# Optimization experiments

Hardware: AMD Instinct MI355X
Metric: run time of the kernel (lower is better)

Reference implementation:

```python
import jax, jax.numpy as jnp
import numpy as np

B, T, C, N = 4, 1024, 1024, 64
H = C // N
# dims = [max(32, 32*round(fac*C**p/32))] per module formula for C=1024
D_W, D_A, D_V, D_G = 64, 64, 32, 160
GN_EPS = 0.00064


def setup_inputs() -> dict:
    key = jax.random.key(0)
    keys = iter(jax.random.split(key, 40))

    def rn(shape, s=0.02):
        return jax.random.normal(next(keys), shape, jnp.float32) * s

    return {
        "x": jax.random.normal(next(keys), (B, T, C), jnp.float32),
        "v_first": jax.random.normal(next(keys), (B, T, C), jnp.float32),
        "x_r": rn((1, 1, C), 0.5), "x_w": rn((1, 1, C), 0.5), "x_k": rn((1, 1, C), 0.5),
        "x_v": rn((1, 1, C), 0.5), "x_a": rn((1, 1, C), 0.5), "x_g": rn((1, 1, C), 0.5),
        "w0": rn((1, 1, C), 0.5) - 1.0, "w1": rn((C, D_W)), "w2": rn((D_W, C)),
        "a0": rn((1, 1, C), 0.5), "a1": rn((C, D_A)), "a2": rn((D_A, C)),
        "v0p": rn((1, 1, C), 0.5), "v1": rn((C, D_V)), "v2": rn((D_V, C)),
        "g1": rn((C, D_G)), "g2": rn((D_G, C)),
        "k_k": rn((1, 1, C), 0.2) + 0.8, "k_a": rn((1, 1, C), 0.2) + 1.0,
        "r_k": rn((H, N), 0.5),
        "W_r": rn((C, C)), "W_k": rn((C, C)), "W_v": rn((C, C)), "W_o": rn((C, C)),
        "gn_w": jnp.ones((C,), jnp.float32), "gn_b": jnp.zeros((C,), jnp.float32),
    }


def _group_norm(x2, wgt, bias):
    # torch GroupNorm(H groups, C channels) on [B*T, C]: normalize each N-chunk
    xg = x2.reshape(x2.shape[0], H, N)
    mu = xg.mean(-1, keepdims=True)
    var = ((xg - mu) ** 2).mean(-1, keepdims=True)  # biased var, as torch
    xn = (xg - mu) * jax.lax.rsqrt(var + GN_EPS)
    return xn.reshape(x2.shape) * wgt + bias


def rwkv7_recurrence(r, w, k, v, a, b):
    # RWKV-7 chunked-cuda semantics (wind_rwkv naive reference), all [B,T,H,N];
    # w is the per-channel decay exp(-exp(w_raw)) in (0,1).
    # state s: [B,H,N,N], s[i,j] ~ value_i x key_j
    # s_t = s_{t-1} * diag(w_t) + (s_{t-1} @ a_t) outer b_t + v_t outer k_t
    # y_t = s_t @ r_t
    def step(s, inp):
        r_t, w_t, k_t, v_t, a_t, b_t = inp  # each [B,H,N]
        sa = jnp.einsum('bhij,bhj->bhi', s, a_t)
        s = (s * w_t[:, :, None, :]
             + sa[..., None] * b_t[:, :, None, :]
             + v_t[..., None] * k_t[:, :, None, :])
        y = jnp.einsum('bhij,bhj->bhi', s, r_t)
        return s, y

    xs = tuple(jnp.swapaxes(t, 0, 1) for t in (r, w, k, v, a, b))  # [T,B,H,N]
    s0 = jnp.zeros((r.shape[0], r.shape[2], r.shape[3], r.shape[3]), r.dtype)
    _, ys = jax.lax.scan(step, s0, xs)
    return jnp.swapaxes(ys, 0, 1)  # [B,T,H,N]


def reference(x, v_first, x_r, x_w, x_k, x_v, x_a, x_g, w0, w1, w2, a0, a1, a2,
              v0p, v1, v2, g1, g2, k_k, k_a, r_k, W_r, W_k, W_v, W_o, gn_w, gn_b):
    Bx, Tx, Cx = x.shape
    # F.pad(x, (0,0,1,-1)): shift tokens right by one, zero at t=0
    last_x = jnp.concatenate([jnp.zeros_like(x[:, :1]), x[:, :-1]], axis=1)
    dx = last_x - x
    xr, xw, xk, xv, xa, xg = (x + m * dx for m in (x_r, x_w, x_k, x_v, x_a, x_g))
    r = xr @ W_r.T
    w = -jax.nn.softplus(-w0 - jnp.tanh(xw @ w1) @ w2) - 0.5
    k = xk @ W_k.T
    v = xv @ W_v.T
    v = v + (v_first - v) * jax.nn.sigmoid(v0p + (xv @ v1) @ v2)
    a = jax.nn.sigmoid(a0 + (xa @ a1) @ a2)
    g = jax.nn.sigmoid(xg @ g1) @ g2
    kk = k * k_k
    k = k * (1.0 + (a - 1.0) * k_a)
    rs, ws, ks, vs, kks, aa = (t.reshape(Bx, Tx, H, N) for t in (r, w, k, v, kk, a))
    # F.normalize(kk, dim=-1) with eps clamp 1e-12
    kks = kks / jnp.maximum(jnp.linalg.norm(kks, axis=-1, keepdims=True), 1e-12)
    wdec = jnp.exp(-jnp.exp(ws))
    y = rwkv7_recurrence(rs, wdec, ks, vs, kks, -kks * aa)  # [B,T,H,N]
    yn = _group_norm(y.reshape(Bx * Tx, Cx), gn_w, gn_b).reshape(Bx, Tx, Cx)
    yn = yn + ((rs * ks * r_k).sum(-1, keepdims=True) * vs).reshape(Bx, Tx, Cx)
    return (yn * g) @ W_o.T
```

## Files before the change

kernel.cpp:

```cpp
#include <hip/hip_runtime.h>
#include <hip/hip_bf16.h>
#include <math.h>


using bf16 = __hip_bfloat16;
typedef __attribute__((ext_vector_type(8))) short bf16x8;
typedef __attribute__((ext_vector_type(4))) float f32x4;

#define DEVINL __device__ __forceinline__

DEVINL float b2f(bf16 v) { return __bfloat162float(v); }
DEVINL bf16 f2b(float f) { return __float2bfloat16(f); }
DEVINL float sigm(float x) { return 1.f / (1.f + __expf(-x)); }
DEVINL float bfbits2f(unsigned short s) { return __uint_as_float(((unsigned)s) << 16); }
DEVINL float lo16(unsigned u) { return __uint_as_float(u << 16); }
DEVINL float hi16(unsigned u) { return __uint_as_float(u & 0xffff0000u); }
DEVINL float ldin(const void* p, size_t i, int fl) {
  return fl ? ((const float*)p)[i] : b2f(((const bf16*)p)[i]);
}

DEVINL void g2lds16(const void* g, void* l) {
  __builtin_amdgcn_global_load_lds(
      (__attribute__((address_space(1))) void*)(g),
      (__attribute__((address_space(3))) void*)(l), 16, 0, 0);
}

template<int CTRL>
DEVINL float dpp_add(float x) {
  int t = __builtin_amdgcn_update_dpp(0, __float_as_int(x), CTRL, 0xf, 0xf, true);
  return x + __int_as_float(t);
}
DEVINL float rowsum16(float x) {
  x = dpp_add<0x121>(x);
  x = dpp_add<0x122>(x);
  x = dpp_add<0x124>(x);
  x = dpp_add<0x128>(x);
  return x;
}

DEVINL size_t stream_sb(int row, int h) {
  return ((size_t)((row >> 10) * 16 + h) * 1024 + (row & 1023)) * 512;
}

__global__ void detect_kernel(const unsigned* __restrict__ x, int* __restrict__ flag) {
  __shared__ int cnt[4];
  int tid = threadIdx.x;
  unsigned w = x[tid];
  float v = fabsf(bfbits2f((unsigned short)(w & 0xffffu)));
  bool plaus = (v >= 1e-4f && v <= 16.f);
  unsigned long long m = __ballot(plaus);
  if ((tid & 63) == 0) cnt[tid >> 6] = __popcll(m);
  __syncthreads();
  if (tid == 0) *flag = (cnt[0] + cnt[1] + cnt[2] + cnt[3] < 128) ? 1 : 0;
}

__global__ __launch_bounds__(256)
void prep_kernel(const void* __restrict__ x,
    const void* mr, const void* mw, const void* mk,
    const void* mv, const void* ma, const void* mg,
    const void* W_r, const void* W_k, const void* W_v, const void* W_o,
    bf16* cWr, bf16* cWk, bf16* cWv, bf16* cWo,
    const void* w1, const void* w2, const void* a1, const void* a2,
    const void* v1, const void* v2, const void* g1, const void* g2,
    bf16* w1t, bf16* w2t, bf16* a1t, bf16* a2t,
    bf16* v1t, bf16* v2t, bf16* g1t, bf16* g2t,
    const int* __restrict__ flag,
    bf16* oxr, bf16* oxw, bf16* oxk, bf16* oxv, bf16* oxa, bf16* oxg)
{
  int fl = *flag;
  int bx = blockIdx.x;
  if (bx < 16384) {
    size_t idx = (size_t)bx * 256 + threadIdx.x;
    int c = (int)(idx & 1023);
    int t = (int)((idx >> 10) & 1023);
    float xc = ldin(x, idx, fl);
    float px = (t == 0) ? 0.f : ldin(x, idx - 1024, fl);
    float dx = px - xc;
    oxr[idx] = f2b(xc + ldin(mr, c, fl) * dx);
    oxw[idx] = f2b(xc + ldin(mw, c, fl) * dx);
    oxk[idx] = f2b(xc + ldin(mk, c, fl) * dx);
    oxv[idx] = f2b(xc + ldin(mv, c, fl) * dx);
    oxa[idx] = f2b(xc + ldin(ma, c, fl) * dx);
    oxg[idx] = f2b(xc + ldin(mg, c, fl) * dx);
  } else if (bx < 32768) {
    int g = (bx - 16384) * 256 + threadIdx.x;
    int seg = g >> 20, i = g & 1048575;
    const void* s = seg == 0 ? W_r : seg == 1 ? W_k : seg == 2 ? W_v : W_o;
    bf16* d = seg == 0 ? cWr : seg == 1 ? cWk : seg == 2 ? cWv : cWo;
    d[i] = fl ? f2b(((const float*)s)[i]) : ((const bf16*)s)[i];
  } else {
    int idx = (bx - 32768) * 256 + threadIdx.x;
    if (idx >= 655360) return;
    const int ends[8] = {65536, 131072, 196608, 262144, 294912, 327680, 491520, 655360};
    const int Ks[8] = {1024, 64, 1024, 64, 1024, 32, 1024, 160};
    const int Nd[8] = {64, 1024, 64, 1024, 32, 1024, 160, 1024};
    const void* srcs[8] = {w1, w2, a1, a2, v1, v2, g1, g2};
    bf16* dsts[8] = {w1t, w2t, a1t, a2t, v1t, v2t, g1t, g2t};
    int seg = 0, start = 0;
#pragma unroll
    for (int s2 = 0; s2 < 7; s2++)
      if (idx >= ends[s2]) { seg = s2 + 1; start = ends[s2]; }
    int local = idx - start;
    int K = Ks[seg], N = Nd[seg];
    int k = local / N, n = local - k * N;
    dsts[seg][(size_t)n * K + k] = f2b(ldin(srcs[seg], local, fl));
  }
}

template<typename Epi>
DEVINL void gemm_core(const bf16* __restrict__ A, const bf16* __restrict__ Bt,
                      int K, int Brows, int m0, int n0, Epi&& epi)
{
  __shared__ short As[128 * 32];
  __shared__ short Bs[128 * 32];
  const int tid = threadIdx.x;
  const int wid = tid >> 6, lane = tid & 63;
  const int wr = (wid >> 1) * 64, wc = (wid & 1) * 64;

  f32x4 acc[4][4] = {};

  const int lrow = lane >> 2;
  const int lcol = (lane & 3) * 8;
  int arow0 = m0 + (wid * 2 + 0) * 16 + lrow;
  int arow1 = m0 + (wid * 2 + 1) * 16 + lrow;
  int brow0 = n0 + (wid * 2 + 0) * 16 + lrow; if (brow0 >= Brows) brow0 = Brows - 1;
  int brow1 = n0 + (wid * 2 + 1) * 16 + lrow; if (brow1 >= Brows) brow1 = Brows - 1;

  const short* Ag = (const short*)A;
  const short* Bg = (const short*)Bt;

  for (int kk = 0; kk < K; kk += 32) {
    __syncthreads();
    g2lds16(Ag + (size_t)arow0 * K + kk + lcol, As + (wid * 2 + 0) * 512);
    g2lds16(Ag + (size_t)arow1 * K + kk + lcol, As + (wid * 2 + 1) * 512);
    g2lds16(Bg + (size_t)brow0 * K + kk + lcol, Bs + (wid * 2 + 0) * 512);
    g2lds16(Bg + (size_t)brow1 * K + kk + lcol, Bs + (wid * 2 + 1) * 512);
    __syncthreads();
    bf16x8 af[4], bfr[4];
#pragma unroll
    for (int mi = 0; mi < 4; mi++)
      af[mi] = *(const bf16x8*)(As + (wr + mi * 16 + (lane & 15)) * 32 + (lane >> 4) * 8);
#pragma unroll
    for (int ni = 0; ni < 4; ni++)
      bfr[ni] = *(const bf16x8*)(Bs + (wc + ni * 16 + (lane & 15)) * 32 + (lane >> 4) * 8);
#pragma unroll
    for (int mi = 0; mi < 4; mi++)
#pragma unroll
      for (int ni = 0; ni < 4; ni++)
        acc[mi][ni] = __builtin_amdgcn_mfma_f32_16x16x32_bf16(af[mi], bfr[ni], acc[mi][ni], 0, 0, 0);
  }

  const int cl0 = lane & 15, r0 = (lane >> 4) * 4;
#pragma unroll
  for (int mi = 0; mi < 4; mi++)
#pragma unroll
    for (int ni = 0; ni < 4; ni++) {
      int col = n0 + wc + ni * 16 + cl0;
#pragma unroll
      for (int rr = 0; rr < 4; rr++)
        epi(m0 + wr + mi * 16 + r0 + rr, col, acc[mi][ni][rr]);
    }
}

__global__ __launch_bounds__(256)
void stage1_kernel(const bf16* xw, const bf16* xa, const bf16* xv, const bf16* xg,
                   const bf16* w1t, const bf16* a1t, const bf16* v1t, const bf16* g1t,
                   bf16* hw, bf16* ha, bf16* hv, bf16* hg)
{
  int y = blockIdx.y;
  int seg = (y <= 2) ? y : 3;
  int n0 = (y == 4) ? 128 : 0;
  const bf16* A  = seg == 0 ? xw  : seg == 1 ? xa  : seg == 2 ? xv  : xg;
  const bf16* Bt = seg == 0 ? w1t : seg == 1 ? a1t : seg == 2 ? v1t : g1t;
  int NS         = seg == 0 ? 64  : seg == 1 ? 64  : seg == 2 ? 32  : 160;
  bf16* out      = seg == 0 ? hw  : seg == 1 ? ha  : seg == 2 ? hv  : hg;
  gemm_core(A, Bt, 1024, NS, blockIdx.x * 128, n0, [&](int row, int col, float f) {
    if (col >= NS) return;
    if (seg == 0) f = tanhf(f);
    else if (seg == 3) f = sigm(f);
    out[(size_t)row * NS + col] = f2b(f);
  });
}

__global__ __launch_bounds__(256)
void bigrkv_kernel(const bf16* xr, const bf16* xk, const bf16* xv,
                   const bf16* cWr, const bf16* cWk, const bf16* cWv,
                   bf16* __restrict__ STR)
{
  int z = blockIdx.z;
  const bf16* A  = z == 0 ? xr  : z == 1 ? xk  : xv;
  const bf16* Bt = z == 0 ? cWr : z == 1 ? cWk : cWv;
  gemm_core(A, Bt, 1024, 1024, blockIdx.x * 128, blockIdx.y * 128,
            [&](int row, int col, float f) {
    size_t sb = stream_sb(row, col >> 6);
    int n = col & 63;
    size_t off = (z == 2) ? (sb + 256 + n) : (sb + n * 4 + z);
    STR[off] = f2b(f);
  });
}

__global__ __launch_bounds__(256)
void stage2_kernel(const bf16* hw, const bf16* ha, const bf16* hv, const bf16* hg,
                   const bf16* w2t, const bf16* a2t, const bf16* v2t, const bf16* g2t,
                   bf16* __restrict__ STR, float* __restrict__ STRf, float* __restrict__ G,
                   const void* w0, const void* a0, const void* v0p, const void* vfirst,
                   const int* __restrict__ flag)
{
  int fl = *flag;
  int z = blockIdx.z;
  const bf16* A  = z == 0 ? hw  : z == 1 ? ha  : z == 2 ? hv  : hg;
  const bf16* Bt = z == 0 ? w2t : z == 1 ? a2t : z == 2 ? v2t : g2t;
  int K          = z == 0 ? 64  : z == 1 ? 64  : z == 2 ? 32  : 160;
  gemm_core(A, Bt, K, 1024, blockIdx.x * 128, blockIdx.y * 128,
            [&](int row, int col, float f) {
    int n = col & 63;
    if (z == 0) {
      float zz = -(ldin(w0, col, fl) + f);
      float sp = fmaxf(zz, 0.f) + __logf(1.f + __expf(-fabsf(zz)));
      STRf[stream_sb(row, col >> 6) / 2 + 160 + n] = __expf(-__expf(-sp - 0.5f));
    } else if (z == 1) {
      STR[stream_sb(row, col >> 6) + n * 4 + 2] = f2b(sigm(ldin(a0, col, fl) + f));
    } else if (z == 2) {
      float sg = sigm(ldin(v0p, col, fl) + f);
      size_t pa = stream_sb(row, col >> 6) + 256 + n;
      float vr = b2f(STR[pa]);
      float vf = ldin(vfirst, (size_t)row * 1024 + col, fl);
      STR[pa] = f2b(vr + (vf - vr) * sg);
    } else {
      G[(size_t)row * 1024 + col] = f;
    }
  });
}

__global__ __launch_bounds__(256)
void post_kernel(bf16* __restrict__ STR, const void* __restrict__ kkw,
                 const void* __restrict__ kaw, const int* __restrict__ flag) {
  int fl = *flag;
  int slot = blockIdx.x * 4 + (threadIdx.x >> 6);
  int tg = slot >> 4, h = slot & 15;
  int n = threadIdx.x & 63, c = h * 64 + n;
  size_t sb = stream_sb(tg, h);
  float kraw = b2f(STR[sb + n * 4 + 1]);
  float asig = b2f(STR[sb + n * 4 + 2]);
  float kk = kraw * ldin(kkw, c, fl);
  float ss = kk * kk;
  ss += __shfl_xor(ss, 1);  ss += __shfl_xor(ss, 2);  ss += __shfl_xor(ss, 4);
  ss += __shfl_xor(ss, 8);  ss += __shfl_xor(ss, 16); ss += __shfl_xor(ss, 32);
  float kkn = kk / fmaxf(sqrtf(ss), 1e-12f);
  STR[sb + n * 4 + 2] = f2b(kkn);
  STR[sb + n * 4 + 3] = f2b(-kkn * asig);
  STR[sb + n * 4 + 1] = f2b(kraw * (1.f + (asig - 1.f) * ldin(kaw, c, fl)));
}

#define CH 8
__global__ __launch_bounds__(64, 1)
void recur_kernel(const char* __restrict__ STR, float* __restrict__ Y) {
  int blk = blockIdx.x;
  int bh = blk & 63, sib = blk >> 6;
  int b = bh >> 4, h = bh & 15;
  int lane = threadIdx.x;
  int jq = lane & 15, rl = lane >> 4;
  int i = sib * 4 + rl;

  const char* rec = STR + (size_t)bh * (1024 * 1024);
  const char* prk = rec + jq * 32;
  const char* pv  = rec + 512 + i * 2;
  const char* pw  = rec + 640 + jq * 16;
  float* yout = Y + (size_t)b * 1024 * 1024 + h * 64 + i;

  uint4 am0[CH], am1[CH]; float4 awv[CH]; unsigned short avu[CH];
  uint4 bm0[CH], bm1[CH]; float4 bwv[CH]; unsigned short bvu[CH];

  float S0 = 0.f, S1 = 0.f, S2 = 0.f, S3 = 0.f;

#define RLOAD(M0, M1, WV, VU, TT) do { \
    size_t _o = (size_t)(TT) * 1024; \
    M0 = *(const uint4*)(prk + _o); \
    M1 = *(const uint4*)(prk + _o + 16); \
    WV = *(const float4*)(pw + _o); \
    VU = *(const unsigned short*)(pv + _o); \
  } while (0)

#define RSTEP(M0, M1, WV, VU, TT) do { \
    float vi = bfbits2f(VU); \
    float rx = lo16(M0.x), kx = hi16(M0.x), ax = lo16(M0.y), bxx = hi16(M0.y); \
    float ry = lo16(M0.z), ky = hi16(M0.z), ay = lo16(M0.w), byy = hi16(M0.w); \
    float rz = lo16(M1.x), kz = hi16(M1.x), az = lo16(M1.y), bzz = hi16(M1.y); \
    float rw2 = lo16(M1.z), kw2 = hi16(M1.z), aw2 = lo16(M1.w), bww = hi16(M1.w); \
    float sa = (S0 * ax + S1 * ay) + (S2 * az + S3 * aw2); \
    sa = rowsum16(sa); \
    S0 = S0 * WV.x + (sa * bxx + vi * kx); \
    S1 = S1 * WV.y + (sa * byy + vi * ky); \
    S2 = S2 * WV.z + (sa * bzz + vi * kz); \
    S3 = S3 * WV.w + (sa * bww + vi * kw2); \
    float yy = (S0 * rx + S1 * ry) + (S2 * rz + S3 * rw2); \
    yy = rowsum16(yy); \
    if (jq == 0) yout[(size_t)(TT) * 1024] = yy; \
  } while (0)

#pragma unroll
  for (int d = 0; d < CH; ++d) RLOAD(am0[d], am1[d], awv[d], avu[d], d);

  for (int t0 = 0; t0 < 1024; t0 += 2 * CH) {
#pragma unroll
    for (int d = 0; d < CH; ++d) RLOAD(bm0[d], bm1[d], bwv[d], bvu[d], t0 + CH + d);
#pragma unroll
    for (int d = 0; d < CH; ++d) RSTEP(am0[d], am1[d], awv[d], avu[d], t0 + d);
#pragma unroll
    for (int d = 0; d < CH; ++d) RLOAD(am0[d], am1[d], awv[d], avu[d], t0 + 2 * CH + d);
#pragma unroll
    for (int d = 0; d < CH; ++d) RSTEP(bm0[d], bm1[d], bwv[d], bvu[d], t0 + CH + d);
  }
#undef RLOAD
#undef RSTEP
}

__global__ __launch_bounds__(256)
void gn_kernel(const float* __restrict__ Y, const bf16* __restrict__ STR,
               const float* __restrict__ G,
               const void* __restrict__ gw, const void* __restrict__ gb,
               const void* __restrict__ rk, const int* __restrict__ flag,
               bf16* __restrict__ Z)
{
  int fl = *flag;
  int slot = blockIdx.x * 4 + (threadIdx.x >> 6);
  int tg = slot >> 4, h = slot & 15;
  int n = threadIdx.x & 63, c = h * 64 + n;
  size_t sb = stream_sb(tg, h);
  float y = Y[(size_t)tg * 1024 + c];
  float rr = b2f(STR[sb + n * 4]), kf = b2f(STR[sb + n * 4 + 1]), vv = b2f(STR[sb + 256 + n]);
  float s1 = y, s2 = y * y, s3 = rr * kf * ldin(rk, c, fl);
#pragma unroll
  for (int m = 1; m < 64; m <<= 1) {
    s1 += __shfl_xor(s1, m);
    s2 += __shfl_xor(s2, m);
    s3 += __shfl_xor(s3, m);
  }
  float mu = s1 * 0.015625f;
  float var = s2 * 0.015625f - mu * mu;
  float xn = (y - mu) * rsqrtf(var + 0.00064f);
  float yn = xn * ldin(gw, c, fl) + ldin(gb, c, fl);
  yn += s3 * vv;
  Z[(size_t)tg * 1024 + c] = f2b(yn * G[(size_t)tg * 1024 + c]);
}

__global__ __launch_bounds__(256)
void outgemm_kernel(const bf16* Z, const bf16* cWo,
                    float* oF, bf16* oB, const int* __restrict__ flag)
{
  int fl = *flag;
  gemm_core(Z, cWo, 1024, 1024, blockIdx.x * 128, blockIdx.y * 128,
            [&](int row, int col, float f) {
    if (fl) oF[(size_t)row * 1024 + col] = f;
    else    oB[(size_t)row * 1024 + col] = f2b(f);
  });
}

extern "C" void kernel_launch(void* const* d_in, const int* in_sizes, int n_in,
                              void* d_out, int out_size, void* d_ws, size_t ws_size,
                              hipStream_t stream)
{
  const void* x      = d_in[0];
  const void* vfirst = d_in[1];
  const void* m_r = d_in[2];  const void* m_w = d_in[3];
  const void* m_k = d_in[4];  const void* m_v = d_in[5];
  const void* m_a = d_in[6];  const void* m_g = d_in[7];
  const void* w0  = d_in[8];  const void* w1  = d_in[9];  const void* w2  = d_in[10];
  const void* a0  = d_in[11]; const void* a1  = d_in[12]; const void* a2  = d_in[13];
  const void* v0p = d_in[14]; const void* v1  = d_in[15]; const void* v2  = d_in[16];
  const void* g1  = d_in[17]; const void* g2  = d_in[18];
  const void* k_k = d_in[19]; const void* k_a = d_in[20]; const void* r_k = d_in[21];
  const void* W_r = d_in[22]; const void* W_k = d_in[23];
  const void* W_v = d_in[24]; const void* W_o = d_in[25];
  const void* gnw = d_in[26]; const void* gnb = d_in[27];
  (void)in_sizes; (void)n_in; (void)out_size; (void)ws_size;

  char* ws = (char*)d_ws;
  size_t off = 0;
  auto alloc = [&](size_t bytes) -> void* {
    void* p = ws + off; off += (bytes + 255) & ~(size_t)255; return p;
  };
  const size_t BTC2 = (size_t)4096 * 1024 * 2;
  int*  flag = (int*)alloc(256);
  bf16* cWr = (bf16*)alloc((size_t)1048576 * 2);
  bf16* cWk = (bf16*)alloc((size_t)1048576 * 2);
  bf16* cWv = (bf16*)alloc((size_t)1048576 * 2);
  bf16* cWo = (bf16*)alloc((size_t)1048576 * 2);
  bf16* w1t = (bf16*)alloc((size_t)65536 * 2);
  bf16* w2t = (bf16*)alloc((size_t)65536 * 2);
  bf16* a1t = (bf16*)alloc((size_t)65536 * 2);
  bf16* a2t = (bf16*)alloc((size_t)65536 * 2);
  bf16* v1t = (bf16*)alloc((size_t)32768 * 2);
  bf16* v2t = (bf16*)alloc((size_t)32768 * 2);
  bf16* g1t = (bf16*)alloc((size_t)163840 * 2);
  bf16* g2t = (bf16*)alloc((size_t)163840 * 2);
  bf16* xr = (bf16*)alloc(BTC2);
  bf16* xw = (bf16*)alloc(BTC2);
  bf16* xk = (bf16*)alloc(BTC2);
  bf16* xv = (bf16*)alloc(BTC2);
  bf16* xa = (bf16*)alloc(BTC2);
  bf16* xg = (bf16*)alloc(BTC2);
  char* STR = (char*)alloc((size_t)64 * 1024 * 1024 + 16384);
  bf16* hw  = (bf16*)alloc((size_t)4096 * 64 * 2);
  bf16* ha  = (bf16*)alloc((size_t)4096 * 64 * 2);
  bf16* hv  = (bf16*)alloc((size_t)4096 * 32 * 2);
  bf16* hg  = (bf16*)alloc((size_t)4096 * 160 * 2);
  float* G = (float*)xr;
  float* Y = (float*)xk;
  bf16*  Z = xa;

  detect_kernel<<<1, 256, 0, stream>>>((const unsigned*)x, flag);
  prep_kernel<<<35328, 256, 0, stream>>>(
      x, m_r, m_w, m_k, m_v, m_a, m_g,
      W_r, W_k, W_v, W_o, cWr, cWk, cWv, cWo,
      w1, w2, a1, a2, v1, v2, g1, g2,
      w1t, w2t, a1t, a2t, v1t, v2t, g1t, g2t,
      flag, xr, xw, xk, xv, xa, xg);

  stage1_kernel<<<dim3(32, 5), 256, 0, stream>>>(xw, xa, xv, xg,
                                                 w1t, a1t, v1t, g1t, hw, ha, hv, hg);
  bigrkv_kernel<<<dim3(32, 8, 3), 256, 0, stream>>>(xr, xk, xv, cWr, cWk, cWv, (bf16*)STR);
  stage2_kernel<<<dim3(32, 8, 4), 256, 0, stream>>>(hw, ha, hv, hg,
                                                    w2t, a2t, v2t, g2t,
                                                    (bf16*)STR, (float*)STR, G,
                                                    w0, a0, v0p, vfirst, flag);
  post_kernel<<<16384, 256, 0, stream>>>((bf16*)STR, k_k, k_a, flag);
  recur_kernel<<<1024, 64, 0, stream>>>(STR, Y);
  gn_kernel<<<16384, 256, 0, stream>>>(Y, (bf16*)STR, G, gnw, gnb, r_k, flag, Z);
  outgemm_kernel<<<dim3(32, 8), 256, 0, stream>>>(Z, cWo, (float*)d_out, (bf16*)d_out, flag);
}
```

Measured before the change: 692.3 us.

## Stage recurrence inputs through LDS with async global-to-LDS double buffering

The recurrence kernel now copies each 1 KB per-timestep record into a double-buffered LDS area with global_load_lds, waiting on vmcnt before reading the current chunk. The r/k/a/b slot layout in the stream buffer is permuted so that each lane's 16-byte LDS read is contiguous, and the producer and consumer kernels are updated to match. The aim is to hide global-memory latency on the serial time loop and to cut register use from the large prefetch arrays. The risks are the hand-written waitcnt encoding being wrong, which would break correctness, and extra LDS-read latency on the critical path.

```diff
diff --git a/kernel.cpp b/kernel.cpp
--- a/kernel.cpp
+++ b/kernel.cpp
@@ -25,6 +25,12 @@
       (__attribute__((address_space(3))) void*)(l), 16, 0, 0);
 }
 
+DEVINL void wait_vmcnt8() {
+  __asm__ volatile("" ::: "memory");
+  __builtin_amdgcn_s_waitcnt(0x0F78);
+  __asm__ volatile("" ::: "memory");
+}
+
 template<int CTRL>
 DEVINL float dpp_add(float x) {
   int t = __builtin_amdgcn_update_dpp(0, __float_as_int(x), CTRL, 0xf, 0xf, true);
@@ -40,6 +46,10 @@
 
 DEVINL size_t stream_sb(int row, int h) {
   return ((size_t)((row >> 10) * 16 + h) * 1024 + (row & 1023)) * 512;
+}
+DEVINL size_t slotoff(int n, int s) {
+  int u = n * 4 + s;
+  return (size_t)(((u >> 3) & 1) * 128 + ((u >> 4) << 3) + (u & 7));
 }
 
 __global__ void detect_kernel(const unsigned* __restrict__ x, int* __restrict__ flag) {
@@ -194,7 +204,7 @@
             [&](int row, int col, float f) {
     size_t sb = stream_sb(row, col >> 6);
     int n = col & 63;
-    size_t off = (z == 2) ? (sb + 256 + n) : (sb + n * 4 + z);
+    size_t off = (z == 2) ? (sb + 256 + n) : (sb + slotoff(n, z));
     STR[off] = f2b(f);
   });
 }
@@ -219,7 +229,7 @@
       float sp = fmaxf(zz, 0.f) + __logf(1.f + __expf(-fabsf(zz)));
       STRf[stream_sb(row, col >> 6) / 2 + 160 + n] = __expf(-__expf(-sp - 0.5f));
     } else if (z == 1) {
-      STR[stream_sb(row, col >> 6) + n * 4 + 2] = f2b(sigm(ldin(a0, col, fl) + f));
+      STR[stream_sb(row, col >> 6) + slotoff(n, 2)] = f2b(sigm(ldin(a0, col, fl) + f));
     } else if (z == 2) {
       float sg = sigm(ldin(v0p, col, fl) + f);
       size_t pa = stream_sb(row, col >> 6) + 256 + n;
@@ -240,21 +250,22 @@
   int tg = slot >> 4, h = slot & 15;
   int n = threadIdx.x & 63, c = h * 64 + n;
   size_t sb = stream_sb(tg, h);
-  float kraw = b2f(STR[sb + n * 4 + 1]);
-  float asig = b2f(STR[sb + n * 4 + 2]);
+  float kraw = b2f(STR[sb + slotoff(n, 1)]);
+  float asig = b2f(STR[sb + slotoff(n, 2)]);
   float kk = kraw * ldin(kkw, c, fl);
   float ss = kk * kk;
   ss += __shfl_xor(ss, 1);  ss += __shfl_xor(ss, 2);  ss += __shfl_xor(ss, 4);
   ss += __shfl_xor(ss, 8);  ss += __shfl_xor(ss, 16); ss += __shfl_xor(ss, 32);
   float kkn = kk / fmaxf(sqrtf(ss), 1e-12f);
-  STR[sb + n * 4 + 2] = f2b(kkn);
-  STR[sb + n * 4 + 3] = f2b(-kkn * asig);
-  STR[sb + n * 4 + 1] = f2b(kraw * (1.f + (asig - 1.f) * ldin(kaw, c, fl)));
+  STR[sb + slotoff(n, 2)] = f2b(kkn);
+  STR[sb + slotoff(n, 3)] = f2b(-kkn * asig);
+  STR[sb + slotoff(n, 1)] = f2b(kraw * (1.f + (asig - 1.f) * ldin(kaw, c, fl)));
 }
 
 #define CH 8
 __global__ __launch_bounds__(64, 1)
 void recur_kernel(const char* __restrict__ STR, float* __restrict__ Y) {
+  __shared__ __align__(16) char lds[2 * CH * 1024];
   int blk = blockIdx.x;
   int bh = blk & 63, sib = blk >> 6;
   int b = bh >> 4, h = bh & 15;
@@ -262,27 +273,31 @@
   int jq = lane & 15, rl = lane >> 4;
   int i = sib * 4 + rl;
 
-  const char* rec = STR + (size_t)bh * (1024 * 1024);
-  const char* prk = rec + jq * 32;
-  const char* pv  = rec + 512 + i * 2;
-  const char* pw  = rec + 640 + jq * 16;
+  const char* gb = STR + (size_t)bh * (1024 * 1024) + lane * 16;
   float* yout = Y + (size_t)b * 1024 * 1024 + h * 64 + i;
 
-  uint4 am0[CH], am1[CH]; float4 awv[CH]; unsigned short avu[CH];
-  uint4 bm0[CH], bm1[CH]; float4 bwv[CH]; unsigned short bvu[CH];
+  const char* pa = lds + jq * 16;
+  const char* pb = lds + 256 + jq * 16;
+  const char* pv = lds + 512 + i * 2;
+  const char* pw = lds + 640 + jq * 16;
+
+#pragma unroll
+  for (int d = 0; d < CH; ++d)
+    g2lds16(gb + (size_t)d * 1024, lds + d * 1024);
 
   float S0 = 0.f, S1 = 0.f, S2 = 0.f, S3 = 0.f;
-
-#define RLOAD(M0, M1, WV, VU, TT) do { \
-    size_t _o = (size_t)(TT) * 1024; \
-    M0 = *(const uint4*)(prk + _o); \
-    M1 = *(const uint4*)(prk + _o + 16); \
-    WV = *(const float4*)(pw + _o); \
-    VU = *(const unsigned short*)(pv + _o); \
+  uint4 m0r[2], m1r[2]; float4 wvr[2]; unsigned short vur[2];
+
+#define RLOAD(BK, SO) do { \
+    m0r[BK] = *(const uint4*)(pa + (SO)); \
+    m1r[BK] = *(const uint4*)(pb + (SO)); \
+    wvr[BK] = *(const float4*)(pw + (SO)); \
+    vur[BK] = *(const unsigned short*)(pv + (SO)); \
   } while (0)
 
-#define RSTEP(M0, M1, WV, VU, TT) do { \
-    float vi = bfbits2f(VU); \
+#define RSTEP(BK, TT) do { \
+    uint4 M0 = m0r[BK], M1 = m1r[BK]; float4 WV = wvr[BK]; \
+    float vi = bfbits2f(vur[BK]); \
     float rx = lo16(M0.x), kx = hi16(M0.x), ax = lo16(M0.y), bxx = hi16(M0.y); \
     float ry = lo16(M0.z), ky = hi16(M0.z), ay = lo16(M0.w), byy = hi16(M0.w); \
     float rz = lo16(M1.x), kz = hi16(M1.x), az = lo16(M1.y), bzz = hi16(M1.y); \
@@ -298,18 +313,20 @@
     if (jq == 0) yout[(size_t)(TT) * 1024] = yy; \
   } while (0)
 
-#pragma unroll
-  for (int d = 0; d < CH; ++d) RLOAD(am0[d], am1[d], awv[d], avu[d], d);
-
-  for (int t0 = 0; t0 < 1024; t0 += 2 * CH) {
-#pragma unroll
-    for (int d = 0; d < CH; ++d) RLOAD(bm0[d], bm1[d], bwv[d], bvu[d], t0 + CH + d);
-#pragma unroll
-    for (int d = 0; d < CH; ++d) RSTEP(am0[d], am1[d], awv[d], avu[d], t0 + d);
-#pragma unroll
-    for (int d = 0; d < CH; ++d) RLOAD(am0[d], am1[d], awv[d], avu[d], t0 + 2 * CH + d);
-#pragma unroll
-    for (int d = 0; d < CH; ++d) RSTEP(bm0[d], bm1[d], bwv[d], bvu[d], t0 + CH + d);
+  for (int t0 = 0; t0 < 1024; t0 += CH) {
+    int cur = (t0 >> 3) & 1;
+    int cbase = cur * (CH * 1024);
+    char* bufn = lds + (cur ^ 1) * (CH * 1024);
+#pragma unroll
+    for (int d = 0; d < CH; ++d)
+      g2lds16(gb + (size_t)(t0 + CH + d) * 1024, bufn + d * 1024);
+    wait_vmcnt8();
+    RLOAD(0, cbase);
+#pragma unroll
+    for (int d = 0; d < CH; ++d) {
+      if (d + 1 < CH) RLOAD((d + 1) & 1, cbase + (d + 1) * 1024);
+      RSTEP(d & 1, t0 + d);
+    }
   }
 #undef RLOAD
 #undef RSTEP
@@ -328,7 +345,9 @@
   int n = threadIdx.x & 63, c = h * 64 + n;
   size_t sb = stream_sb(tg, h);
   float y = Y[(size_t)tg * 1024 + c];
-  float rr = b2f(STR[sb + n * 4]), kf = b2f(STR[sb + n * 4 + 1]), vv = b2f(STR[sb + 256 + n]);
+  float rr = b2f(STR[sb + slotoff(n, 0)]);
+  float kf = b2f(STR[sb + slotoff(n, 1)]);
+  float vv = b2f(STR[sb + 256 + n]);
   float s1 = y, s2 = y * y, s3 = rr * kf * ldin(rk, c, fl);
 #pragma unroll
   for (int m = 1; m < 64; m <<= 1) {
```

Measured after the change: 571.3 us. 1.21x faster.
